# Kernel tuning notes

Measured on AMD Instinct MI355X. Metric: run time of the kernel, lower is better.

Reference implementation:

```python
import jax, jax.numpy as jnp
import numpy as np

B, N, DIM, H, DH, M = 2, 2048, 1024, 16, 64, 512
INNER = H * DH  # 1024
KV = M + 1 + N  # xl mem + null kv + sequence = 2561


def rotate_half(x):
    x1, x2 = jnp.split(x, 2, axis=-1)
    return jnp.concatenate([-x2, x1], axis=-1)


def apply_rotary_pos_emb(pos, t):
    return t * jnp.cos(pos) + rotate_half(t) * jnp.sin(pos)


def setup_inputs() -> dict:
    key = jax.random.key(0)
    ks = jax.random.split(key, 8)
    return {
        "x": jax.random.normal(ks[0], (B, N, DIM), jnp.float32),
        "rotary_q": jax.random.uniform(ks[1], (N, DH), jnp.float32) * 6.28,
        "rotary_k": jax.random.uniform(ks[2], (KV, DH), jnp.float32) * 6.28,
        "xl_memories": jax.random.normal(ks[3], (2, B, H, M, DH), jnp.float32) * 0.02,
        "Wq": jax.random.normal(ks[4], (DIM, INNER), jnp.float32) * 0.02,
        "Wkv": jax.random.normal(ks[5], (DIM, 2 * INNER), jnp.float32) * 0.02,
        "Wout": jax.random.normal(ks[6], (INNER, INNER), jnp.float32) * 0.02,
        "null_kv": jax.random.normal(ks[7], (2, H, DH), jnp.float32),
    }


def reference(x, rotary_q, rotary_k, xl_memories, Wq, Wkv, Wout, null_kv):
    # QKV projections (no bias, matching keras Dense(use_bias=False))
    q = (x @ Wq).reshape(B, N, H, DH).transpose(0, 2, 1, 3)  # b h n d
    k, v = jnp.split(x @ Wkv, 2, axis=-1)
    k = k.reshape(B, N, H, DH).transpose(0, 2, 1, 3)
    v = v.reshape(B, N, H, DH).transpose(0, 2, 1, 3)

    # prepend learned null key/value (1 token)
    nk = jnp.broadcast_to(null_kv[0][None, :, None, :], (B, H, 1, DH))
    nv = jnp.broadcast_to(null_kv[1][None, :, None, :], (B, H, 1, DH))
    k = jnp.concatenate([nk, k], axis=2)
    v = jnp.concatenate([nv, v], axis=2)

    next_xl_memories = jnp.stack([k, v])  # [2, b, h, 1+n, d]

    # prepend XL memories along key axis
    k = jnp.concatenate([xl_memories[0], k], axis=2)  # b h kv d
    v = jnp.concatenate([xl_memories[1], v], axis=2)

    # inline rotary embedding on q and (full) k
    q = apply_rotary_pos_emb(rotary_q, q)
    k = apply_rotary_pos_emb(rotary_k, k)

    # causal attention with bottom-right aligned mask (mem/null tokens visible)
    scale = DH ** -0.5
    sim = jnp.einsum('bhid,bhjd->bhij', q, k) * scale  # b h n kv
    i = jnp.arange(N)[:, None]
    j = jnp.arange(KV)[None, :]
    causal_ok = j <= (i + (KV - N))
    sim = jnp.where(causal_ok, sim, jnp.finfo(sim.dtype).min)
    attn = jax.nn.softmax(sim, axis=-1)
    out = jnp.einsum('bhij,bhjd->bhid', attn, v)  # b h n d

    out = out.transpose(0, 2, 1, 3).reshape(B, N, INNER)
    return out @ Wout, next_xl_memories
```

## Files before the change

### kernel.cpp

```cpp
#include <hip/hip_runtime.h>
#include <hip/hip_bf16.h>


typedef short v8s __attribute__((ext_vector_type(8)));
typedef float v4f __attribute__((ext_vector_type(4)));

__device__ __forceinline__ float bf2f(unsigned short x) {
  return __uint_as_float(((unsigned)x) << 16);
}
__device__ __forceinline__ unsigned short f2bf(float f) {
  unsigned u = __float_as_uint(f);
  u += 0x7FFFu + ((u >> 16) & 1u);
  return (unsigned short)(u >> 16);
}

#if __has_builtin(__builtin_amdgcn_exp2f)
#define EXP2(x) __builtin_amdgcn_exp2f(x)
#else
#define EXP2(x) exp2f(x)
#endif

__device__ __forceinline__ void gld_lds16(const void* g, void* l) {
  __builtin_amdgcn_global_load_lds(
      (const __attribute__((address_space(1))) unsigned int*)g,
      (__attribute__((address_space(3))) unsigned int*)l, 16, 0, 0);
}

__device__ __forceinline__ unsigned pk_bf16(float lo, float hi) {
  union { __hip_bfloat162 h; unsigned u; } cv;
  cv.h = __float22bfloat162_rn(make_float2(lo, hi));
  return cv.u;
}

__global__ __launch_bounds__(256) void cvt_bf16(
    const float* __restrict__ S, unsigned short* __restrict__ D, int n4)
{
  const int i = blockIdx.x * 256 + threadIdx.x;
  if (i < n4) {
    const float4 v = ((const float4*)S)[i];
    ushort4 o;
    o.x = f2bf(v.x); o.y = f2bf(v.y); o.z = f2bf(v.z); o.w = f2bf(v.w);
    ((ushort4*)D)[i] = o;
  }
}

template <typename CT>
__global__ __launch_bounds__(256, 2) void gemm_bf16(
    const unsigned short* __restrict__ A,
    const unsigned short* __restrict__ WT,
    CT* __restrict__ C,
    int K, int ldc)
{
  __shared__ unsigned short As[128 * 64];
  __shared__ unsigned short Bs[128 * 64];
  const int tid  = threadIdx.x;
  const int wave = tid >> 6, lane = tid & 63;
  const int l15  = lane & 15, quad = lane >> 4;
  const int wm   = wave >> 1, wn = wave & 1;
  const int row0 = blockIdx.x * 128, col0 = blockIdx.y * 128;
  const int lrow = lane >> 3;
  const int gsw  = (lane & 7) ^ lrow;

  v4f acc[4][4];
  const v4f vzero = {0.f, 0.f, 0.f, 0.f};
#pragma unroll
  for (int i = 0; i < 4; ++i)
#pragma unroll
    for (int j = 0; j < 4; ++j) acc[i][j] = vzero;

  for (int k0 = 0; k0 < K; k0 += 64) {
    __syncthreads();
#pragma unroll
    for (int ro = 0; ro < 4; ++ro) {
      const int chunk = wave * 4 + ro;
      const int arow  = chunk * 8 + lrow;
      gld_lds16(A  + (size_t)(row0 + arow) * K + k0 + gsw * 8, As + chunk * 512);
      gld_lds16(WT + (size_t)(col0 + arow) * K + k0 + gsw * 8, Bs + chunk * 512);
    }
    __syncthreads();

    v8s af[4][2], bf[4][2];
#pragma unroll
    for (int tm = 0; tm < 4; ++tm) {
      const int r = wm * 64 + tm * 16 + l15;
#pragma unroll
      for (int kk = 0; kk < 2; ++kk) {
        const int slot = (kk * 4 + quad) ^ (r & 7);
        af[tm][kk] = *(const v8s*)(As + r * 64 + slot * 8);
      }
    }
#pragma unroll
    for (int tn = 0; tn < 4; ++tn) {
      const int r = wn * 64 + tn * 16 + l15;
#pragma unroll
      for (int kk = 0; kk < 2; ++kk) {
        const int slot = (kk * 4 + quad) ^ (r & 7);
        bf[tn][kk] = *(const v8s*)(Bs + r * 64 + slot * 8);
      }
    }
#pragma unroll
    for (int kk = 0; kk < 2; ++kk)
#pragma unroll
      for (int tm = 0; tm < 4; ++tm)
#pragma unroll
        for (int tn = 0; tn < 4; ++tn)
          acc[tm][tn] = __builtin_amdgcn_mfma_f32_16x16x32_bf16(
              af[tm][kk], bf[tn][kk], acc[tm][tn], 0, 0, 0);
  }

#pragma unroll
  for (int tm = 0; tm < 4; ++tm)
#pragma unroll
    for (int tn = 0; tn < 4; ++tn)
#pragma unroll
      for (int r = 0; r < 4; ++r) {
        const int row = row0 + wm * 64 + tm * 16 + quad * 4 + r;
        const int col = col0 + wn * 64 + tn * 16 + l15;
        if constexpr (sizeof(CT) == 2)
          C[(size_t)row * ldc + col] = (CT)f2bf(acc[tm][tn][r]);
        else
          C[(size_t)row * ldc + col] = (CT)acc[tm][tn][r];
      }
}

__global__ __launch_bounds__(256) void transpose_wt(
    const float* __restrict__ S0,
    const float* __restrict__ S1,
    int c0, int c1, int K,
    unsigned short* __restrict__ D)
{
  __shared__ float T[64][65];
  const int k0 = blockIdx.x * 64, n0 = blockIdx.y * 64;
  const int tid = threadIdx.x;
#pragma unroll
  for (int ro = 0; ro < 4; ++ro) {
    const int idx = ro * 256 + tid;
    const int kr = idx >> 4, ch = idx & 15;
    const int n = n0 + ch * 4;
    float4 val;
    if (n < c0) val = *(const float4*)(S0 + (size_t)(k0 + kr) * c0 + n);
    else        val = *(const float4*)(S1 + (size_t)(k0 + kr) * c1 + (n - c0));
    T[kr][ch * 4 + 0] = val.x; T[kr][ch * 4 + 1] = val.y;
    T[kr][ch * 4 + 2] = val.z; T[kr][ch * 4 + 3] = val.w;
  }
  __syncthreads();
#pragma unroll
  for (int ro = 0; ro < 2; ++ro) {
    const int idx = ro * 256 + tid;
    const int nl = idx >> 3, ch = idx & 7;
    __align__(16) unsigned short tmp[8];
#pragma unroll
    for (int e = 0; e < 8; ++e) tmp[e] = f2bf(T[ch * 8 + e][nl]);
    *(uint4*)(D + (size_t)(n0 + nl) * K + k0 + ch * 8) = *(const uint4*)tmp;
  }
}

__global__ __launch_bounds__(256) void assemble(
    const unsigned short* __restrict__ QKV,
    const float* __restrict__ rq,
    const float* __restrict__ rk,
    const float* __restrict__ xlm,
    const float* __restrict__ nkv,
    unsigned short* __restrict__ Qrot,
    unsigned short* __restrict__ Kf,
    unsigned short* __restrict__ Vn,
    float* __restrict__ nxl)
{
  const int gw = blockIdx.x * 4 + (threadIdx.x >> 6);
  const int d  = threadIdx.x & 63;
  const int RK = 32 * 2561;
  const int RQ = 32 * 2048;
  if (gw < RK) {
    const int bh = gw / 2561;
    const int j  = gw - bh * 2561;
    const int b  = bh >> 4, h = bh & 15;
    float kx, vx;
    if (j < 512) {
      const size_t i0 = (((size_t)(b * 16 + h)) * 512 + j) * 64 + d;
      kx = xlm[i0];
      vx = xlm[1048576 + i0];
    } else if (j == 512) {
      kx = nkv[h * 64 + d];
      vx = nkv[1024 + h * 64 + d];
    } else {
      const size_t rowb = ((size_t)(b * 2048 + (j - 513))) * 3072;
      kx = bf2f(QKV[rowb + 1024 + h * 64 + d]);
      vx = bf2f(QKV[rowb + 2048 + h * 64 + d]);
    }
    Vn[(((size_t)bh) * 2561 + j) * 64 + d] = f2bf(vx);
    if (j >= 512) {
      const size_t o0 = (((size_t)(b * 16 + h)) * 2049 + (j - 512)) * 64 + d;
      nxl[o0] = kx;
      nxl[4196352 + o0] = vx;
    }
    const float ang = rk[j * 64 + d];
    const float cs = __cosf(ang), sn = __sinf(ang);
    const float part = __shfl_xor(kx, 32);
    const float kr = kx * cs + (d < 32 ? -part : part) * sn;
    Kf[(((size_t)bh) * 2624 + j) * 64 + d] = f2bf(kr);
  } else if (gw < RK + RQ) {
    const int g2 = gw - RK;
    const int bh = g2 >> 11, n = g2 & 2047;
    const int b  = bh >> 4, h = bh & 15;
    const float qx = bf2f(QKV[((size_t)(b * 2048 + n)) * 3072 + h * 64 + d]);
    const float ang = rq[n * 64 + d];
    const float cs = __cosf(ang), sn = __sinf(ang);
    const float part = __shfl_xor(qx, 32);
    const float qr = qx * cs + (d < 32 ? -part : part) * sn;
    Qrot[(((size_t)bh) * 2048 + n) * 64 + d] = f2bf(qr * 0.18033688f);
  } else {
    const int g3 = gw - RK - RQ;
    const int bh = g3 / 63;
    const int jj = 2561 + (g3 - bh * 63);
    Kf[(((size_t)bh) * 2624 + jj) * 64 + d] = 0;
  }
}

__global__ __launch_bounds__(256) void transpose_v(
    const unsigned short* __restrict__ Vn,
    unsigned short* __restrict__ VTp)
{
  __shared__ unsigned short T[64][72];
  const int j0 = blockIdx.x * 64;
  const int bh = blockIdx.y;
  const int tid = threadIdx.x;
#pragma unroll
  for (int ro = 0; ro < 2; ++ro) {
    const int idx = ro * 256 + tid;
    const int jr = idx >> 3, ch = idx & 7;
    uint4 val = make_uint4(0, 0, 0, 0);
    if (j0 + jr < 2561)
      val = *(const uint4*)(Vn + (((size_t)bh) * 2561 + j0 + jr) * 64 + ch * 8);
    *(uint4*)(&T[jr][ch * 8]) = val;
  }
  __syncthreads();
#pragma unroll
  for (int ro = 0; ro < 2; ++ro) {
    const int idx = ro * 256 + tid;
    const int dl = idx >> 3, ch = idx & 7;
    __align__(16) unsigned short tmp[8];
#pragma unroll
    for (int e = 0; e < 8; ++e) {
      const int kappa = ch * 8 + e;
      const int sig = ((kappa & 31) >> 1) + ((kappa & 1) << 4) + (kappa & 32);
      tmp[e] = T[sig][dl];
    }
    *(uint4*)(VTp + (((size_t)bh) * 64 + dl) * 2624 + j0 + ch * 8) = *(const uint4*)tmp;
  }
}

__global__ __launch_bounds__(256, 4) void attn_fa(
    const unsigned short* __restrict__ Qr,
    const unsigned short* __restrict__ Kf,
    const unsigned short* __restrict__ VTp,
    unsigned short* __restrict__ Ao)
{
  const int bh = blockIdx.y;
  const int qb = 31 - (int)((blockIdx.x + blockIdx.y) & 31);
  const int b = bh >> 4, h = bh & 15;
  __shared__ unsigned short Ps[4 * 16 * 72];
  __shared__ unsigned short Ks[64 * 72];
  __shared__ unsigned short Vs[64 * 72];
  const int tid = threadIdx.x;
  const int wave = tid >> 6, lane = tid & 63;
  const int l15 = lane & 15, quad = lane >> 4;
  const v4f vzero = {0.f, 0.f, 0.f, 0.f};

  v8s qf[2];
  {
    const unsigned short* Qg =
        Qr + (((size_t)bh) * 2048 + qb * 64 + wave * 16 + l15) * 64;
    qf[0] = *(const v8s*)(Qg + quad * 8);
    qf[1] = *(const v8s*)(Qg + 32 + quad * 8);
  }
  unsigned short* Pw = Ps + wave * 16 * 72;

  v4f O[4], Ol;
#pragma unroll
  for (int dt = 0; dt < 4; ++dt) O[dt] = vzero;
  Ol = vzero;
  const short one_bf = (short)0x3F80;
  const v8s ones = {one_bf, one_bf, one_bf, one_bf,
                    one_bf, one_bf, one_bf, one_bf};

  const unsigned short* Kg0 = Kf + (size_t)bh * 2624 * 64;
  const unsigned short* Vg0 = VTp + (size_t)bh * 64 * 2624;
  const int ntiles = (qb + 10 <= 41) ? (qb + 10) : 41;
  const int tfast  = qb + 7;

  const int srow = tid >> 3, sch = tid & 7;
  const int srow1 = srow + 32;

#define PREFETCH(t, ka, kb, va, vb)                                          \
  {                                                                          \
    const int j0p = (t) * 64;                                                \
    ka = *(const uint4*)(Kg0 + (size_t)(j0p + srow) * 64 + sch * 8);         \
    va = *(const uint4*)(Vg0 + (size_t)srow * 2624 + j0p + sch * 8);         \
    kb = *(const uint4*)(Kg0 + (size_t)(j0p + srow1) * 64 + sch * 8);        \
    vb = *(const uint4*)(Vg0 + (size_t)srow1 * 2624 + j0p + sch * 8);        \
  }
#define STAGE(ka, kb, va, vb)                                                \
  {                                                                          \
    *(uint4*)(Ks + srow * 72 + sch * 8) = ka;                                \
    *(uint4*)(Vs + srow * 72 + sch * 8) = va;                                \
    *(uint4*)(Ks + srow1 * 72 + sch * 8) = kb;                               \
    *(uint4*)(Vs + srow1 * 72 + sch * 8) = vb;                               \
  }

  auto compute_tile = [&](int j0, bool masked) {
    v4f s[4];
#pragma unroll
    for (int jt = 0; jt < 4; ++jt) {
      const v8s kfr0 = *(const v8s*)(Ks + (jt * 16 + l15) * 72 + quad * 8);
      const v8s kfr1 = *(const v8s*)(Ks + (jt * 16 + l15) * 72 + 32 + quad * 8);
      v4f c = vzero;
      c = __builtin_amdgcn_mfma_f32_16x16x32_bf16(qf[0], kfr0, c, 0, 0, 0);
      c = __builtin_amdgcn_mfma_f32_16x16x32_bf16(qf[1], kfr1, c, 0, 0, 0);
      s[jt] = c;
    }

    if (masked) {
      const int ibase = qb * 64 + wave * 16 + quad * 4 + 513;
#pragma unroll
      for (int jt = 0; jt < 4; ++jt) {
        const int jg = j0 + jt * 16 + l15;
#pragma unroll
        for (int r = 0; r < 4; ++r)
          s[jt][r] = (jg <= ibase + r) ? s[jt][r] : -1e30f;
      }
    }

#pragma unroll
    for (int r = 0; r < 4; ++r) {
      const unsigned d0 = pk_bf16(EXP2(s[0][r]), EXP2(s[1][r]));
      const unsigned d1 = pk_bf16(EXP2(s[2][r]), EXP2(s[3][r]));
      unsigned short* pr = Pw + (quad * 4 + r) * 72 + 2 * l15;
      *(unsigned*)(pr)      = d0;
      *(unsigned*)(pr + 32) = d1;
    }
    __asm__ volatile("s_waitcnt lgkmcnt(0)" ::: "memory");
    __builtin_amdgcn_sched_barrier(0);

    v8s pf[2];
    pf[0] = *(const v8s*)(Pw + l15 * 72 + quad * 8);
    pf[1] = *(const v8s*)(Pw + l15 * 72 + 32 + quad * 8);
#pragma unroll
    for (int dt = 0; dt < 4; ++dt) {
      const v8s vf0 = *(const v8s*)(Vs + (dt * 16 + l15) * 72 + quad * 8);
      const v8s vf1 = *(const v8s*)(Vs + (dt * 16 + l15) * 72 + 32 + quad * 8);
      v4f c = O[dt];
      c = __builtin_amdgcn_mfma_f32_16x16x32_bf16(pf[0], vf0, c, 0, 0, 0);
      c = __builtin_amdgcn_mfma_f32_16x16x32_bf16(pf[1], vf1, c, 0, 0, 0);
      O[dt] = c;
    }
    Ol = __builtin_amdgcn_mfma_f32_16x16x32_bf16(pf[0], ones, Ol, 0, 0, 0);
    Ol = __builtin_amdgcn_mfma_f32_16x16x32_bf16(pf[1], ones, Ol, 0, 0, 0);
  };

  uint4 k0a, k0b, v0a, v0b, k1a, k1b, v1a, v1b;
  PREFETCH(0, k0a, k0b, v0a, v0b);
  for (int t = 0; t < ntiles; t += 2) {
    __syncthreads();
    STAGE(k0a, k0b, v0a, v0b);
    if (t + 1 < ntiles) PREFETCH(t + 1, k1a, k1b, v1a, v1b);
    __syncthreads();
    compute_tile(t * 64, t > tfast);
    if (t + 1 >= ntiles) break;
    __syncthreads();
    STAGE(k1a, k1b, v1a, v1b);
    if (t + 2 < ntiles) PREFETCH(t + 2, k0a, k0b, v0a, v0b);
    __syncthreads();
    compute_tile((t + 1) * 64, (t + 1) > tfast);
  }
#undef PREFETCH
#undef STAGE

#pragma unroll
  for (int r = 0; r < 4; ++r) {
    const float linv = 1.0f / Ol[r];
    const int n = qb * 64 + wave * 16 + quad * 4 + r;
    const size_t rowbase = ((size_t)b * 2048 + n) * 1024 + h * 64;
#pragma unroll
    for (int dt = 0; dt < 4; ++dt)
      Ao[rowbase + dt * 16 + l15] = f2bf(O[dt][r] * linv);
  }
}

extern "C" void kernel_launch(void* const* d_in, const int* in_sizes, int n_in,
                              void* d_out, int out_size, void* d_ws, size_t ws_size,
                              hipStream_t stream)
{
  const float* x    = (const float*)d_in[0];
  const float* rq   = (const float*)d_in[1];
  const float* rk   = (const float*)d_in[2];
  const float* xlm  = (const float*)d_in[3];
  const float* Wq   = (const float*)d_in[4];
  const float* Wkv  = (const float*)d_in[5];
  const float* Wout = (const float*)d_in[6];
  const float* nkv  = (const float*)d_in[7];
  float* out = (float*)d_out;
  float* nxl = out + 4194304;
  char* ws = (char*)d_ws;
  unsigned short* QKV   = (unsigned short*)(ws + 0);
  unsigned short* xbf   = (unsigned short*)(ws + 25165824);
  unsigned short* Ao    = (unsigned short*)(ws + 25165824);
  unsigned short* WqkvT = (unsigned short*)(ws + 33554432);
  unsigned short* WoutT = (unsigned short*)(ws + 39845888);
  unsigned short* Qrot  = (unsigned short*)(ws + 41943040);
  unsigned short* Kf    = (unsigned short*)(ws + 50331648);
  unsigned short* Vn    = (unsigned short*)(ws + 61079552);
  unsigned short* VTp   = (unsigned short*)(ws + 71569408);

  cvt_bf16<<<4096, 256, 0, stream>>>(x, xbf, 1048576);
  transpose_wt<<<dim3(16, 48), 256, 0, stream>>>(Wq, Wkv, 1024, 2048, 1024, WqkvT);
  transpose_wt<<<dim3(16, 16), 256, 0, stream>>>(Wout, Wout, 1024, 1024, 1024, WoutT);
  gemm_bf16<unsigned short><<<dim3(32, 24), 256, 0, stream>>>(xbf, WqkvT, QKV, 1024, 3072);
  assemble<<<37376, 256, 0, stream>>>(QKV, rq, rk, xlm, nkv, Qrot, Kf, Vn, nxl);
  transpose_v<<<dim3(41, 32), 256, 0, stream>>>(Vn, VTp);
  attn_fa<<<dim3(32, 32), 256, 0, stream>>>(Qrot, Kf, VTp, Ao);
  gemm_bf16<float><<<dim3(32, 8), 256, 0, stream>>>(Ao, WoutT, out, 1024, 1024);
}
```

Measured before the change: 236.9 us.

## Keep softmax probabilities in registers via transposed QK MFMA and double-buffer K/V LDS

The QK^T MFMA now takes K as the A operand, so each lane holds scores in the layout the PV MFMA expects for its P operand. The exponentiated probabilities are packed straight into registers, removing the per-tile LDS write/read round trip and its waitcnt. The V-transpose permutation is changed to match the new key ordering. K/V staging now uses two LDS buffers with one barrier per tile instead of two, at the cost of more shared memory per block.

```diff
diff --git a/kernel.cpp b/kernel.cpp
--- a/kernel.cpp
+++ b/kernel.cpp
@@ -242,7 +242,7 @@
 #pragma unroll
     for (int e = 0; e < 8; ++e) {
       const int kappa = ch * 8 + e;
-      const int sig = ((kappa & 31) >> 1) + ((kappa & 1) << 4) + (kappa & 32);
+      const int sig = (kappa & 32) + ((e & 4) << 2) + ((ch & 3) << 2) + (e & 3);
       tmp[e] = T[sig][dl];
     }
     *(uint4*)(VTp + (((size_t)bh) * 64 + dl) * 2624 + j0 + ch * 8) = *(const uint4*)tmp;
@@ -258,9 +258,8 @@
   const int bh = blockIdx.y;
   const int qb = 31 - (int)((blockIdx.x + blockIdx.y) & 31);
   const int b = bh >> 4, h = bh & 15;
-  __shared__ unsigned short Ps[4 * 16 * 72];
-  __shared__ unsigned short Ks[64 * 72];
-  __shared__ unsigned short Vs[64 * 72];
+  __shared__ unsigned short Ks[2][64 * 72];
+  __shared__ unsigned short Vs[2][64 * 72];
   const int tid = threadIdx.x;
   const int wave = tid >> 6, lane = tid & 63;
   const int l15 = lane & 15, quad = lane >> 4;
@@ -273,7 +272,7 @@
     qf[0] = *(const v8s*)(Qg + quad * 8);
     qf[1] = *(const v8s*)(Qg + 32 + quad * 8);
   }
-  unsigned short* Pw = Ps + wave * 16 * 72;
+  const int qbase = qb * 64 + wave * 16 + l15 + 513;
 
   v4f O[4], Ol;
 #pragma unroll
@@ -290,8 +289,9 @@
 
   const int srow = tid >> 3, sch = tid & 7;
   const int srow1 = srow + 32;
-
-#define PREFETCH(t, ka, kb, va, vb)                                          \
+  uint4 ka, kb, va, vb;
+
+#define PREFETCH(t)                                                          \
   {                                                                          \
     const int j0p = (t) * 64;                                                \
     ka = *(const uint4*)(Kg0 + (size_t)(j0p + srow) * 64 + sch * 8);         \
@@ -299,78 +299,71 @@
     kb = *(const uint4*)(Kg0 + (size_t)(j0p + srow1) * 64 + sch * 8);        \
     vb = *(const uint4*)(Vg0 + (size_t)srow1 * 2624 + j0p + sch * 8);        \
   }
-#define STAGE(ka, kb, va, vb)                                                \
+#define STAGE(bi)                                                            \
   {                                                                          \
-    *(uint4*)(Ks + srow * 72 + sch * 8) = ka;                                \
-    *(uint4*)(Vs + srow * 72 + sch * 8) = va;                                \
-    *(uint4*)(Ks + srow1 * 72 + sch * 8) = kb;                               \
-    *(uint4*)(Vs + srow1 * 72 + sch * 8) = vb;                               \
-  }
-
-  auto compute_tile = [&](int j0, bool masked) {
+    *(uint4*)(Ks[bi] + srow * 72 + sch * 8) = ka;                            \
+    *(uint4*)(Vs[bi] + srow * 72 + sch * 8) = va;                            \
+    *(uint4*)(Ks[bi] + srow1 * 72 + sch * 8) = kb;                           \
+    *(uint4*)(Vs[bi] + srow1 * 72 + sch * 8) = vb;                           \
+  }
+
+  auto compute_tile = [&](const unsigned short* Ksb, const unsigned short* Vsb,
+                          int j0, bool masked) {
     v4f s[4];
 #pragma unroll
     for (int jt = 0; jt < 4; ++jt) {
-      const v8s kfr0 = *(const v8s*)(Ks + (jt * 16 + l15) * 72 + quad * 8);
-      const v8s kfr1 = *(const v8s*)(Ks + (jt * 16 + l15) * 72 + 32 + quad * 8);
+      const v8s kfr0 = *(const v8s*)(Ksb + (jt * 16 + l15) * 72 + quad * 8);
+      const v8s kfr1 = *(const v8s*)(Ksb + (jt * 16 + l15) * 72 + 32 + quad * 8);
       v4f c = vzero;
-      c = __builtin_amdgcn_mfma_f32_16x16x32_bf16(qf[0], kfr0, c, 0, 0, 0);
-      c = __builtin_amdgcn_mfma_f32_16x16x32_bf16(qf[1], kfr1, c, 0, 0, 0);
+      c = __builtin_amdgcn_mfma_f32_16x16x32_bf16(kfr0, qf[0], c, 0, 0, 0);
+      c = __builtin_amdgcn_mfma_f32_16x16x32_bf16(kfr1, qf[1], c, 0, 0, 0);
       s[jt] = c;
     }
 
     if (masked) {
-      const int ibase = qb * 64 + wave * 16 + quad * 4 + 513;
 #pragma unroll
       for (int jt = 0; jt < 4; ++jt) {
-        const int jg = j0 + jt * 16 + l15;
+        const int jrow = j0 + jt * 16 + quad * 4;
 #pragma unroll
         for (int r = 0; r < 4; ++r)
-          s[jt][r] = (jg <= ibase + r) ? s[jt][r] : -1e30f;
+          s[jt][r] = (jrow + r <= qbase) ? s[jt][r] : -1e30f;
       }
     }
 
-#pragma unroll
-    for (int r = 0; r < 4; ++r) {
-      const unsigned d0 = pk_bf16(EXP2(s[0][r]), EXP2(s[1][r]));
-      const unsigned d1 = pk_bf16(EXP2(s[2][r]), EXP2(s[3][r]));
-      unsigned short* pr = Pw + (quad * 4 + r) * 72 + 2 * l15;
-      *(unsigned*)(pr)      = d0;
-      *(unsigned*)(pr + 32) = d1;
-    }
-    __asm__ volatile("s_waitcnt lgkmcnt(0)" ::: "memory");
-    __builtin_amdgcn_sched_barrier(0);
-
-    v8s pf[2];
-    pf[0] = *(const v8s*)(Pw + l15 * 72 + quad * 8);
-    pf[1] = *(const v8s*)(Pw + l15 * 72 + 32 + quad * 8);
+    union { unsigned u[4]; v8s s8; } pk0, pk1;
+    pk0.u[0] = pk_bf16(EXP2(s[0][0]), EXP2(s[0][1]));
+    pk0.u[1] = pk_bf16(EXP2(s[0][2]), EXP2(s[0][3]));
+    pk0.u[2] = pk_bf16(EXP2(s[1][0]), EXP2(s[1][1]));
+    pk0.u[3] = pk_bf16(EXP2(s[1][2]), EXP2(s[1][3]));
+    pk1.u[0] = pk_bf16(EXP2(s[2][0]), EXP2(s[2][1]));
+    pk1.u[1] = pk_bf16(EXP2(s[2][2]), EXP2(s[2][3]));
+    pk1.u[2] = pk_bf16(EXP2(s[3][0]), EXP2(s[3][1]));
+    pk1.u[3] = pk_bf16(EXP2(s[3][2]), EXP2(s[3][3]));
+
 #pragma unroll
     for (int dt = 0; dt < 4; ++dt) {
-      const v8s vf0 = *(const v8s*)(Vs + (dt * 16 + l15) * 72 + quad * 8);
-      const v8s vf1 = *(const v8s*)(Vs + (dt * 16 + l15) * 72 + 32 + quad * 8);
+      const v8s vf0 = *(const v8s*)(Vsb + (dt * 16 + l15) * 72 + quad * 8);
+      const v8s vf1 = *(const v8s*)(Vsb + (dt * 16 + l15) * 72 + 32 + quad * 8);
       v4f c = O[dt];
-      c = __builtin_amdgcn_mfma_f32_16x16x32_bf16(pf[0], vf0, c, 0, 0, 0);
-      c = __builtin_amdgcn_mfma_f32_16x16x32_bf16(pf[1], vf1, c, 0, 0, 0);
+      c = __builtin_amdgcn_mfma_f32_16x16x32_bf16(pk0.s8, vf0, c, 0, 0, 0);
+      c = __builtin_amdgcn_mfma_f32_16x16x32_bf16(pk1.s8, vf1, c, 0, 0, 0);
       O[dt] = c;
     }
-    Ol = __builtin_amdgcn_mfma_f32_16x16x32_bf16(pf[0], ones, Ol, 0, 0, 0);
-    Ol = __builtin_amdgcn_mfma_f32_16x16x32_bf16(pf[1], ones, Ol, 0, 0, 0);
+    Ol = __builtin_amdgcn_mfma_f32_16x16x32_bf16(pk0.s8, ones, Ol, 0, 0, 0);
+    Ol = __builtin_amdgcn_mfma_f32_16x16x32_bf16(pk1.s8, ones, Ol, 0, 0, 0);
   };
 
-  uint4 k0a, k0b, v0a, v0b, k1a, k1b, v1a, v1b;
-  PREFETCH(0, k0a, k0b, v0a, v0b);
-  for (int t = 0; t < ntiles; t += 2) {
+  PREFETCH(0);
+  STAGE(0);
+  PREFETCH(1);
+  __syncthreads();
+  for (int t = 0; t < ntiles; ++t) {
+    if (t + 1 < ntiles) {
+      STAGE((t + 1) & 1);
+      if (t + 2 < ntiles) PREFETCH(t + 2);
+    }
+    compute_tile(Ks[t & 1], Vs[t & 1], t * 64, t > tfast);
     __syncthreads();
-    STAGE(k0a, k0b, v0a, v0b);
-    if (t + 1 < ntiles) PREFETCH(t + 1, k1a, k1b, v1a, v1b);
-    __syncthreads();
-    compute_tile(t * 64, t > tfast);
-    if (t + 1 >= ntiles) break;
-    __syncthreads();
-    STAGE(k1a, k1b, v1a, v1b);
-    if (t + 2 < ntiles) PREFETCH(t + 2, k0a, k0b, v0a, v0b);
-    __syncthreads();
-    compute_tile((t + 1) * 64, (t + 1) > tfast);
   }
 #undef PREFETCH
 #undef STAGE
```

Result: faster. 229.5 us (-3.1%).
